# Optimization experiments

Hardware: AMD Instinct MI355X
Metric: run time of the kernel (lower is better)

Reference implementation:

```python
import jax, jax.numpy as jnp
import numpy as np


def setup_inputs() -> dict:
    key = jax.random.key(0)
    k1, k2 = jax.random.split(key)
    N1, N2 = 16384, 16384
    pos1 = jax.random.normal(k1, (N1, 2), dtype=jnp.float32)
    pos2 = jax.random.normal(k2, (N2, 2), dtype=jnp.float32)
    return {"pos1": pos1, "pos2": pos2}


def reference(pos1, pos2):
    # pos1: [N1, 2], pos2: [N2, 2]
    diff = pos1[:, None, :] - pos2[None, :, :]          # [N1, N2, 2]
    dist = jnp.sqrt(jnp.sum(diff * diff, axis=2))       # [N1, N2]
    nearest = jnp.min(dist, axis=1)                     # [N1]
    return jnp.mean(nearest)
```

## Files before the change

kernel.cpp:

```cpp
#include <hip/hip_runtime.h>
#include <math.h>

#define N1 16384
#define N2 16384
#define BLOCK 256
#define PTS 8
#define I_BLOCKS (N1 / (BLOCK * PTS))
#define MAX_SLICE_N 1024
#define UJ 8

__global__ __launch_bounds__(BLOCK)
void nn_partial(const float2* __restrict__ pos1,
                const float2* __restrict__ pos2,
                float* __restrict__ partials,
                unsigned int* __restrict__ ticket,
                int slice_n) {
    __shared__ float4 sp[MAX_SLICE_N];
    const int ib = blockIdx.x;
    const int sl = blockIdx.y;
    const int t  = threadIdx.x;

    if (ib == 0 && sl == 0 && t == 0) *ticket = 0;

    for (int j = t; j < slice_n; j += BLOCK) {
        float2 q = pos2[sl * slice_n + j];
        sp[j] = make_float4(-2.f * q.x, -2.f * q.y,
                            fmaf(q.x, q.x, q.y * q.y), 0.f);
    }
    __syncthreads();

    const int i0 = ib * (BLOCK * PTS) + t;
    float x[PTS], y[PTS], m[PTS];
#pragma unroll
    for (int k = 0; k < PTS; ++k) {
        float2 p = pos1[i0 + k * BLOCK];
        x[k] = p.x;
        y[k] = p.y;
        m[k] = 3.4e38f;
    }

    for (int j = 0; j < slice_n; j += UJ) {
        float4 qb[UJ];
#pragma unroll
        for (int u = 0; u < UJ; ++u) qb[u] = sp[j + u];
#pragma unroll
        for (int u = 0; u < UJ; ++u) {
#pragma unroll
            for (int k = 0; k < PTS; ++k) {
                float g = fmaf(x[k], qb[u].x, fmaf(y[k], qb[u].y, qb[u].z));
                m[k] = fminf(m[k], g);
            }
        }
    }

#pragma unroll
    for (int k = 0; k < PTS; ++k) {
        partials[(size_t)sl * N1 + i0 + k * BLOCK] = m[k];
    }
}

__global__ __launch_bounds__(BLOCK)
void nn_reduce(const float* __restrict__ partials,
               const float2* __restrict__ pos1,
               float* __restrict__ blocksums,
               unsigned int* __restrict__ ticket,
               float* __restrict__ out,
               int slices) {
    const int t = threadIdx.x;
    const int i = blockIdx.x * BLOCK + t;

    float m = 3.4e38f;
    for (int s = 0; s < slices; ++s) {
        m = fminf(m, partials[(size_t)s * N1 + i]);
    }
    float2 p = pos1[i];
    float d2 = fmaxf(fmaf(p.x, p.x, p.y * p.y) + m, 0.f);
    float sum = sqrtf(d2);

    for (int off = 32; off > 0; off >>= 1) {
        sum += __shfl_down(sum, off, 64);
    }
    __shared__ float wsum[BLOCK / 64];
    __shared__ int lastflag;
    if ((t & 63) == 0) wsum[t >> 6] = sum;
    __syncthreads();
    if (t == 0) {
        float s = 0.f;
        for (int w = 0; w < BLOCK / 64; ++w) s += wsum[w];
        blocksums[blockIdx.x] = s;
        __threadfence();
        unsigned int old = atomicAdd(ticket, 1u);
        lastflag = (old == gridDim.x - 1) ? 1 : 0;
    }
    __syncthreads();
    if (lastflag && t < 64) {
        volatile float* vb = (volatile float*)blocksums;
        float v = vb[t];
        for (int off = 32; off > 0; off >>= 1) {
            v += __shfl_down(v, off, 64);
        }
        if (t == 0) out[0] = v / (float)N1;
    }
}

extern "C" void kernel_launch(void* const* d_in, const int* in_sizes, int n_in,
                              void* d_out, int out_size, void* d_ws, size_t ws_size,
                              hipStream_t stream) {
    const float2* pos1 = (const float2*)d_in[0];
    const float2* pos2 = (const float2*)d_in[1];
    float* out = (float*)d_out;
    float* partials = (float*)d_ws;

    const int nblk2 = N1 / BLOCK;
    int slices = 128;
    while (slices > 1 &&
           (size_t)slices * N1 * sizeof(float) + (nblk2 + 1) * sizeof(float) > ws_size)
        slices >>= 1;
    while (N2 / slices > MAX_SLICE_N) slices <<= 1;
    const int slice_n = N2 / slices;

    float* blocksums = partials + (size_t)slices * N1;
    unsigned int* ticket = (unsigned int*)(blocksums + nblk2);

    dim3 grid1(I_BLOCKS, slices);
    nn_partial<<<grid1, BLOCK, 0, stream>>>(pos1, pos2, partials, ticket, slice_n);
    nn_reduce<<<nblk2, BLOCK, 0, stream>>>(partials, pos1, blocksums, ticket, out, slices);
}
```

Measured before the change: 95.41 us.

## Read pos2 directly from global memory and double points per thread

Removes the shared-memory staging of pos2 and the block barrier. Each thread now loads every pos2 point from global memory (broadcast and cached) and computes the -2q and |q|^2 terms inline. Points per thread double to 16 and slices double to 256, which raises reuse per load while keeping the grid size. The cost is redundant per-thread arithmetic on q, scalar global loads inside the inner loop, more register pressure under a 4-block launch bound, and a partials buffer twice as large for the reduce kernel to read.

```diff
diff --git a/kernel.cpp b/kernel.cpp
--- a/kernel.cpp
+++ b/kernel.cpp
@@ -4,30 +4,23 @@
 #define N1 16384
 #define N2 16384
 #define BLOCK 256
-#define PTS 8
+#define PTS 16
 #define I_BLOCKS (N1 / (BLOCK * PTS))
-#define MAX_SLICE_N 1024
-#define UJ 8
+#define SLICES 256
 
-__global__ __launch_bounds__(BLOCK)
+__global__ __launch_bounds__(BLOCK, 4)
 void nn_partial(const float2* __restrict__ pos1,
                 const float2* __restrict__ pos2,
                 float* __restrict__ partials,
                 unsigned int* __restrict__ ticket,
                 int slice_n) {
-    __shared__ float4 sp[MAX_SLICE_N];
     const int ib = blockIdx.x;
     const int sl = blockIdx.y;
     const int t  = threadIdx.x;
 
     if (ib == 0 && sl == 0 && t == 0) *ticket = 0;
 
-    for (int j = t; j < slice_n; j += BLOCK) {
-        float2 q = pos2[sl * slice_n + j];
-        sp[j] = make_float4(-2.f * q.x, -2.f * q.y,
-                            fmaf(q.x, q.x, q.y * q.y), 0.f);
-    }
-    __syncthreads();
+    const float2* __restrict__ q = pos2 + (size_t)sl * slice_n;
 
     const int i0 = ib * (BLOCK * PTS) + t;
     float x[PTS], y[PTS], m[PTS];
@@ -39,17 +32,15 @@
         m[k] = 3.4e38f;
     }
 
-    for (int j = 0; j < slice_n; j += UJ) {
-        float4 qb[UJ];
+#pragma unroll 4
+    for (int j = 0; j < slice_n; ++j) {
+        float2 qj = q[j];
+        float qx = -2.f * qj.x;
+        float qy = -2.f * qj.y;
+        float qz = fmaf(qj.x, qj.x, qj.y * qj.y);
 #pragma unroll
-        for (int u = 0; u < UJ; ++u) qb[u] = sp[j + u];
-#pragma unroll
-        for (int u = 0; u < UJ; ++u) {
-#pragma unroll
-            for (int k = 0; k < PTS; ++k) {
-                float g = fmaf(x[k], qb[u].x, fmaf(y[k], qb[u].y, qb[u].z));
-                m[k] = fminf(m[k], g);
-            }
+        for (int k = 0; k < PTS; ++k) {
+            m[k] = fminf(m[k], fmaf(x[k], qx, fmaf(y[k], qy, qz)));
         }
     }
 
@@ -70,6 +61,7 @@
     const int i = blockIdx.x * BLOCK + t;
 
     float m = 3.4e38f;
+#pragma unroll 8
     for (int s = 0; s < slices; ++s) {
         m = fminf(m, partials[(size_t)s * N1 + i]);
     }
@@ -112,11 +104,10 @@
     float* partials = (float*)d_ws;
 
     const int nblk2 = N1 / BLOCK;
-    int slices = 128;
+    int slices = SLICES;
     while (slices > 1 &&
            (size_t)slices * N1 * sizeof(float) + (nblk2 + 1) * sizeof(float) > ws_size)
         slices >>= 1;
-    while (N2 / slices > MAX_SLICE_N) slices <<= 1;
     const int slice_n = N2 / slices;
 
     float* blocksums = partials + (size_t)slices * N1;
```

Result: slower. 121.3 us (+27.1%).
